# Kernel optimization log

Hardware: AMD Instinct MI355X
Metric: run time of the kernel (lower is better)

Reference implementation:

```python
import jax, jax.numpy as jnp
import numpy as np

N_NODES = 40000
N_EDGES = 640000
IN_DIM = 256
HID = 128
EMB = 128


def _mean_agg(h, src, dst, n):
    # PyG SimpleConv(aggr='mean'): out[i] = mean_{(j->i) in E} h[j]; 0 if no in-edges
    s = jax.ops.segment_sum(h[src], dst, num_segments=n)              # [N, D]
    deg = jax.ops.segment_sum(jnp.ones((src.shape[0],), h.dtype), dst,
                              num_segments=n)                          # [N]
    return s / jnp.maximum(deg, 1.0)[:, None]


def setup_inputs() -> dict:
    key = jax.random.key(0)
    ks = jax.random.split(key, 10)
    scale_in = 1.0 / np.sqrt(IN_DIM)
    scale_mix = 1.0 / np.sqrt(2 * HID)
    scale_out = 1.0 / np.sqrt(HID)
    return {
        "x": jax.random.normal(ks[0], (N_NODES, IN_DIM), dtype=jnp.float32),
        "W_in": jax.random.uniform(ks[1], (IN_DIM, HID), jnp.float32, -scale_in, scale_in),
        "b_in": jnp.zeros((HID,), jnp.float32),
        "W_mix0": jax.random.uniform(ks[2], (2 * HID, HID), jnp.float32, -scale_mix, scale_mix),
        "b_mix0": jnp.zeros((HID,), jnp.float32),
        "W_mix1": jax.random.uniform(ks[3], (2 * HID, HID), jnp.float32, -scale_mix, scale_mix),
        "b_mix1": jnp.zeros((HID,), jnp.float32),
        "W_out": jax.random.uniform(ks[4], (HID, EMB), jnp.float32, -scale_out, scale_out),
        "b_out": jnp.zeros((EMB,), jnp.float32),
        "edge_index": jax.random.randint(ks[5], (2, N_EDGES), 0, N_NODES, dtype=jnp.int64 if jax.config.jax_enable_x64 else jnp.int32),
    }


def reference(x, W_in, b_in, W_mix0, b_mix0, W_mix1, b_mix1, W_out, b_out, edge_index):
    src, dst = edge_index[0], edge_index[1]
    n = x.shape[0]
    # eval mode: dropout is identity
    h = jax.nn.relu(x @ W_in + b_in)                                   # [N, HID]
    for i, (W_mix, b_mix) in enumerate([(W_mix0, b_mix0), (W_mix1, b_mix1)]):
        h1 = _mean_agg(h, src, dst, n)                                 # 1-hop mean
        h2 = _mean_agg(h1, src, dst, n)                                # 2-hop mean
        h = jnp.concatenate([h1, h2], axis=-1) @ W_mix + b_mix         # [N, HID]
        if i != 1:
            h = jax.nn.relu(h)
    return h @ W_out + b_out                                           # [N, EMB]
```

## Files before the change

### kernel.cpp

```cpp
#include <hip/hip_runtime.h>

#define N_NODES 40000
#define N_EDGES 640000
#define IN_DIM 256
#define HID 128
#define NBUCK 313

typedef short bf16x8 __attribute__((ext_vector_type(8)));
typedef float f32x4 __attribute__((ext_vector_type(4)));

__device__ __forceinline__ unsigned short f2bf(float f) {
    unsigned int u = __float_as_uint(f);
    unsigned int r = (u + 0x7FFFu + ((u >> 16) & 1u)) >> 16;
    return (unsigned short)r;
}
__device__ __forceinline__ float bf2f(unsigned short b) {
    return __uint_as_float(((unsigned int)b) << 16);
}


__global__ __launch_bounds__(256) void count_prep(
    const int* __restrict__ dst, int* __restrict__ gbcnt, int E,
    const float* __restrict__ W0, const float* __restrict__ W1,
    const float* __restrict__ W2, const float* __restrict__ W3,
    unsigned short* __restrict__ H0, unsigned short* __restrict__ L0,
    unsigned short* __restrict__ H1, unsigned short* __restrict__ L1,
    unsigned short* __restrict__ H2, unsigned short* __restrict__ L2,
    unsigned short* __restrict__ H3, unsigned short* __restrict__ L3) {
    int bid = blockIdx.x, tid = threadIdx.x;
    if (bid < 157) {
        __shared__ int cnt[NBUCK];
        for (int j = tid; j < NBUCK; j += 256) cnt[j] = 0;
        __syncthreads();
        int base = bid * 4096;
        int lim = min(base + 4096, E);
        for (int i = base + tid; i < lim; i += 256) atomicAdd(&cnt[dst[i] >> 7], 1);
        __syncthreads();
        for (int j = tid; j < NBUCK; j += 256)
            if (cnt[j]) atomicAdd(&gbcnt[j], cnt[j]);
        return;
    }
    int i = (bid - 157) * 256 + tid;
    const float* W;
    unsigned short *H, *L;
    int local;
    if (i < 32768)       { W = W0; H = H0; L = L0; local = i; }
    else if (i < 65536)  { W = W1; H = H1; L = L1; local = i - 32768; }
    else if (i < 98304)  { W = W2; H = H2; L = L2; local = i - 65536; }
    else if (i < 114688) { W = W3; H = H3; L = L3; local = i - 98304; }
    else return;
    int k = local >> 7, c = local & 127;
    float w = W[local];
    unsigned short h = f2bf(w);
    unsigned short l = f2bf(w - bf2f(h));
    int d = (k >> 5) * 4096 + c * 32 + (k & 31);
    H[d] = h;
    L[d] = l;
}


__global__ __launch_bounds__(512) void scan_buckets(const int* __restrict__ gbcnt,
                                                    int* __restrict__ bbase,
                                                    int* __restrict__ bcursor,
                                                    int* __restrict__ row_off) {
    __shared__ int sh[512];
    int tid = threadIdx.x;
    int v = (tid < NBUCK) ? gbcnt[tid] : 0;
    sh[tid] = v;
    __syncthreads();
#pragma unroll
    for (int off = 1; off < 512; off <<= 1) {
        int t = (tid >= off) ? sh[tid - off] : 0;
        __syncthreads();
        sh[tid] += t;
        __syncthreads();
    }
    int excl = sh[tid] - v;
    if (tid < NBUCK) {
        bbase[tid] = excl;
        bcursor[tid] = excl;
    }
    if (tid == NBUCK - 1) bbase[NBUCK] = excl + v;
    if (tid == 0) row_off[N_NODES] = N_EDGES;
}


__global__ __launch_bounds__(256) void scatter_gemm1(
    const int* __restrict__ src, const int* __restrict__ dst,
    int* __restrict__ bcursor, unsigned int* __restrict__ stage, int E,
    const float* __restrict__ x,
    const unsigned short* __restrict__ Bth, const unsigned short* __restrict__ Btl,
    const float* __restrict__ bias, unsigned short* __restrict__ Cbf) {
    int bid = blockIdx.x;
    int tid = threadIdx.x;
    if (bid >= 625) {
        __shared__ int cnt[NBUCK];
        int b2 = bid - 625;
        for (int j = tid; j < NBUCK; j += 256) cnt[j] = 0;
        __syncthreads();
        int base = b2 * 4096;
        int lim = min(base + 4096, E);
        for (int i = base + tid; i < lim; i += 256) atomicAdd(&cnt[dst[i] >> 7], 1);
        __syncthreads();
        for (int j = tid; j < NBUCK; j += 256) {
            int c = cnt[j];
            if (c) cnt[j] = atomicAdd(&bcursor[j], c);
        }
        __syncthreads();
        for (int i = base + tid; i < lim; i += 256) {
            unsigned int d = (unsigned int)dst[i];
            int p = atomicAdd(&cnt[d >> 7], 1);
            stage[p] = (d << 16) | (unsigned int)src[i];
        }
        return;
    }
    __shared__ unsigned short Ah[64 * 32], Al[64 * 32];
    __shared__ unsigned short Bh[128 * 32], Bl[128 * 32];
    int lane = tid & 63, wid = tid >> 6;
    int wr = wid >> 1, wc = wid & 1;
    int row0 = bid * 64;

    f32x4 acc[2][4];
#pragma unroll
    for (int rt = 0; rt < 2; ++rt)
#pragma unroll
        for (int ct = 0; ct < 4; ++ct) acc[rt][ct] = 0.f;

    for (int s = 0; s < 8; ++s) {
        int kbase = s * 32;
#pragma unroll
        for (int i = 0; i < 2; ++i) {
            int cch = tid + i * 256;
            int r = cch >> 3, q = cch & 7;
            float4 v = *(const float4*)&x[(size_t)(row0 + r) * IN_DIM + kbase + q * 4];
            ushort4 hh, ll;
            hh.x = f2bf(v.x); ll.x = f2bf(v.x - bf2f(hh.x));
            hh.y = f2bf(v.y); ll.y = f2bf(v.y - bf2f(hh.y));
            hh.z = f2bf(v.z); ll.z = f2bf(v.z - bf2f(hh.z));
            hh.w = f2bf(v.w); ll.w = f2bf(v.w - bf2f(hh.w));
            *(ushort4*)&Ah[r * 32 + q * 4] = hh;
            *(ushort4*)&Al[r * 32 + q * 4] = ll;
        }
        {
            const float4* sh4 = (const float4*)(Bth + s * 4096);
            const float4* sl4 = (const float4*)(Btl + s * 4096);
            float4* dh4 = (float4*)Bh;
            float4* dl4 = (float4*)Bl;
            dh4[tid] = sh4[tid];
            dh4[tid + 256] = sh4[tid + 256];
            dl4[tid] = sl4[tid];
            dl4[tid + 256] = sl4[tid + 256];
        }
        __syncthreads();

        bf16x8 afh[2], afl[2], bfh[4], bfl[4];
#pragma unroll
        for (int rt = 0; rt < 2; ++rt) {
            int off = (wr * 32 + rt * 16 + (lane & 15)) * 32 + (lane >> 4) * 8;
            afh[rt] = *(const bf16x8*)&Ah[off];
            afl[rt] = *(const bf16x8*)&Al[off];
        }
#pragma unroll
        for (int ct = 0; ct < 4; ++ct) {
            int off = (wc * 64 + ct * 16 + (lane & 15)) * 32 + (lane >> 4) * 8;
            bfh[ct] = *(const bf16x8*)&Bh[off];
            bfl[ct] = *(const bf16x8*)&Bl[off];
        }
#pragma unroll
        for (int rt = 0; rt < 2; ++rt)
#pragma unroll
            for (int ct = 0; ct < 4; ++ct) {
                acc[rt][ct] = __builtin_amdgcn_mfma_f32_16x16x32_bf16(afh[rt], bfh[ct], acc[rt][ct], 0, 0, 0);
                acc[rt][ct] = __builtin_amdgcn_mfma_f32_16x16x32_bf16(afh[rt], bfl[ct], acc[rt][ct], 0, 0, 0);
                acc[rt][ct] = __builtin_amdgcn_mfma_f32_16x16x32_bf16(afl[rt], bfh[ct], acc[rt][ct], 0, 0, 0);
            }
        __syncthreads();
    }

#pragma unroll
    for (int ct = 0; ct < 4; ++ct) {
        int col = wc * 64 + ct * 16 + (lane & 15);
        float bv = bias[col];
#pragma unroll
        for (int rt = 0; rt < 2; ++rt) {
#pragma unroll
            for (int r = 0; r < 4; ++r) {
                int row = row0 + wr * 32 + rt * 16 + (lane >> 4) * 4 + r;
                float v = fmaxf(acc[rt][ct][r] + bv, 0.f);
                Cbf[(size_t)row * 128 + col] = f2bf(v);
            }
        }
    }
}


__global__ __launch_bounds__(256) void finalize_csr(const unsigned int* __restrict__ stage,
                                                    const int* __restrict__ bbase,
                                                    int* __restrict__ row_off,
                                                    int* __restrict__ csr) {
    __shared__ int ncnt[128];
    __shared__ int s2[128];
    int b = blockIdx.x, tid = threadIdx.x;
    int nbase = b << 7;
    int ncount = min(128, N_NODES - nbase);
    int ebase = bbase[b], eend = bbase[b + 1];
    if (tid < 128) ncnt[tid] = 0;
    __syncthreads();
    for (int i = ebase + tid; i < eend; i += 256)
        atomicAdd(&ncnt[(stage[i] >> 16) & 127], 1);
    __syncthreads();
    if (tid < 128) s2[tid] = ncnt[tid];
    __syncthreads();
#pragma unroll
    for (int off = 1; off < 128; off <<= 1) {
        int t = (tid < 128 && tid >= off) ? s2[tid - off] : 0;
        __syncthreads();
        if (tid < 128) s2[tid] += t;
        __syncthreads();
    }
    if (tid < 128) {
        int excl = s2[tid] - ncnt[tid];
        if (tid < ncount) row_off[nbase + tid] = ebase + excl;
        ncnt[tid] = excl;
    }
    __syncthreads();
    for (int i = ebase + tid; i < eend; i += 256) {
        unsigned int ent = stage[i];
        int loc = (ent >> 16) & 127;
        int p = atomicAdd(&ncnt[loc], 1);
        csr[ebase + p] = (int)(ent & 0xFFFFu);
    }
}


__global__ __launch_bounds__(256) void agg_mean_bf(const unsigned short* __restrict__ hbf,
                                                   const int* __restrict__ row_off,
                                                   const int* __restrict__ csr,
                                                   unsigned short* __restrict__ out_bf,
                                                   int N) {
    int node = blockIdx.x * 4 + (threadIdx.x >> 6);
    if (node >= N) return;
    int lane = threadIdx.x & 63;
    int half = lane >> 5;
    int sub = lane & 31;
    int beg = row_off[node], end = row_off[node + 1];
    float4 a0 = make_float4(0.f, 0.f, 0.f, 0.f);
    float4 a1 = make_float4(0.f, 0.f, 0.f, 0.f);
    int e = beg;
    for (; e + 7 < end; e += 8) {
        int s0 = csr[e + half];
        int s1 = csr[e + 2 + half];
        int s2 = csr[e + 4 + half];
        int s3 = csr[e + 6 + half];
        ushort4 u0 = *(const ushort4*)&hbf[(size_t)s0 * HID + sub * 4];
        ushort4 u1 = *(const ushort4*)&hbf[(size_t)s1 * HID + sub * 4];
        ushort4 u2 = *(const ushort4*)&hbf[(size_t)s2 * HID + sub * 4];
        ushort4 u3 = *(const ushort4*)&hbf[(size_t)s3 * HID + sub * 4];
        a0.x += bf2f(u0.x) + bf2f(u2.x);
        a0.y += bf2f(u0.y) + bf2f(u2.y);
        a0.z += bf2f(u0.z) + bf2f(u2.z);
        a0.w += bf2f(u0.w) + bf2f(u2.w);
        a1.x += bf2f(u1.x) + bf2f(u3.x);
        a1.y += bf2f(u1.y) + bf2f(u3.y);
        a1.z += bf2f(u1.z) + bf2f(u3.z);
        a1.w += bf2f(u1.w) + bf2f(u3.w);
    }
    for (; e + half < end; e += 2) {
        int s = csr[e + half];
        ushort4 u = *(const ushort4*)&hbf[(size_t)s * HID + sub * 4];
        a0.x += bf2f(u.x);
        a0.y += bf2f(u.y);
        a0.z += bf2f(u.z);
        a0.w += bf2f(u.w);
    }
    float4 acc;
    acc.x = a0.x + a1.x;
    acc.y = a0.y + a1.y;
    acc.z = a0.z + a1.z;
    acc.w = a0.w + a1.w;
    acc.x += __shfl_xor(acc.x, 32);
    acc.y += __shfl_xor(acc.y, 32);
    acc.z += __shfl_xor(acc.z, 32);
    acc.w += __shfl_xor(acc.w, 32);
    if (half == 0) {
        float inv = 1.0f / fmaxf((float)(end - beg), 1.0f);
        ushort4 ub;
        ub.x = f2bf(acc.x * inv);
        ub.y = f2bf(acc.y * inv);
        ub.z = f2bf(acc.z * inv);
        ub.w = f2bf(acc.w * inv);
        *(ushort4*)&out_bf[(size_t)node * HID + sub * 4] = ub;
    }
}


template <bool RELU>
__global__ __launch_bounds__(256) void gemm_a16(
    const unsigned short* __restrict__ A0, const unsigned short* __restrict__ A1,
    const unsigned short* __restrict__ Bth, const unsigned short* __restrict__ Btl,
    const float* __restrict__ bias, unsigned short* __restrict__ Cbf) {
    __shared__ unsigned short Ab[64 * 32];
    __shared__ unsigned short Bh[128 * 32], Bl[128 * 32];
    int tid = threadIdx.x;
    int lane = tid & 63, wid = tid >> 6;
    int wr = wid >> 1, wc = wid & 1;
    int row0 = blockIdx.x * 64;

    f32x4 acc[2][4];
#pragma unroll
    for (int rt = 0; rt < 2; ++rt)
#pragma unroll
        for (int ct = 0; ct < 4; ++ct) acc[rt][ct] = 0.f;

    for (int s = 0; s < 8; ++s) {
        const unsigned short* Asrc = (s < 4) ? A0 : A1;
        int kbase = (s & 3) * 32;
        {
            int r = tid >> 2, q = (tid & 3) * 8;
            *(float4*)&Ab[r * 32 + q] =
                *(const float4*)&Asrc[(size_t)(row0 + r) * HID + kbase + q];
        }
        {
            const float4* sh4 = (const float4*)(Bth + s * 4096);
            const float4* sl4 = (const float4*)(Btl + s * 4096);
            float4* dh4 = (float4*)Bh;
            float4* dl4 = (float4*)Bl;
            dh4[tid] = sh4[tid];
            dh4[tid + 256] = sh4[tid + 256];
            dl4[tid] = sl4[tid];
            dl4[tid + 256] = sl4[tid + 256];
        }
        __syncthreads();

        bf16x8 af[2], bfh[4], bfl[4];
#pragma unroll
        for (int rt = 0; rt < 2; ++rt) {
            int off = (wr * 32 + rt * 16 + (lane & 15)) * 32 + (lane >> 4) * 8;
            af[rt] = *(const bf16x8*)&Ab[off];
        }
#pragma unroll
        for (int ct = 0; ct < 4; ++ct) {
            int off = (wc * 64 + ct * 16 + (lane & 15)) * 32 + (lane >> 4) * 8;
            bfh[ct] = *(const bf16x8*)&Bh[off];
            bfl[ct] = *(const bf16x8*)&Bl[off];
        }
#pragma unroll
        for (int rt = 0; rt < 2; ++rt)
#pragma unroll
            for (int ct = 0; ct < 4; ++ct) {
                acc[rt][ct] = __builtin_amdgcn_mfma_f32_16x16x32_bf16(af[rt], bfh[ct], acc[rt][ct], 0, 0, 0);
                acc[rt][ct] = __builtin_amdgcn_mfma_f32_16x16x32_bf16(af[rt], bfl[ct], acc[rt][ct], 0, 0, 0);
            }
        __syncthreads();
    }

#pragma unroll
    for (int ct = 0; ct < 4; ++ct) {
        int col = wc * 64 + ct * 16 + (lane & 15);
        float bv = bias[col];
#pragma unroll
        for (int rt = 0; rt < 2; ++rt) {
#pragma unroll
            for (int r = 0; r < 4; ++r) {
                int row = row0 + wr * 32 + rt * 16 + (lane >> 4) * 4 + r;
                float v = acc[rt][ct][r] + bv;
                if (RELU) v = fmaxf(v, 0.f);
                Cbf[(size_t)row * 128 + col] = f2bf(v);
            }
        }
    }
}


__global__ __launch_bounds__(256) void gemm_mix_out(
    const unsigned short* __restrict__ A0, const unsigned short* __restrict__ A1,
    const unsigned short* __restrict__ BmH, const unsigned short* __restrict__ BmL,
    const float* __restrict__ bias_m,
    const unsigned short* __restrict__ BoH, const unsigned short* __restrict__ BoL,
    const float* __restrict__ bias_o, float* __restrict__ out) {
    __shared__ unsigned short Ab[64 * 32];
    __shared__ unsigned short Bh[128 * 32], Bl[128 * 32];
    __shared__ unsigned short AoH[4][64 * 32], AoL[4][64 * 32];
    int tid = threadIdx.x;
    int lane = tid & 63, wid = tid >> 6;
    int wr = wid >> 1, wc = wid & 1;
    int row0 = blockIdx.x * 64;

    f32x4 acc[2][4];
#pragma unroll
    for (int rt = 0; rt < 2; ++rt)
#pragma unroll
        for (int ct = 0; ct < 4; ++ct) acc[rt][ct] = 0.f;

    for (int s = 0; s < 8; ++s) {
        const unsigned short* Asrc = (s < 4) ? A0 : A1;
        int kbase = (s & 3) * 32;
        {
            int r = tid >> 2, q = (tid & 3) * 8;
            *(float4*)&Ab[r * 32 + q] =
                *(const float4*)&Asrc[(size_t)(row0 + r) * HID + kbase + q];
        }
        {
            const float4* sh4 = (const float4*)(BmH + s * 4096);
            const float4* sl4 = (const float4*)(BmL + s * 4096);
            float4* dh4 = (float4*)Bh;
            float4* dl4 = (float4*)Bl;
            dh4[tid] = sh4[tid];
            dh4[tid + 256] = sh4[tid + 256];
            dl4[tid] = sl4[tid];
            dl4[tid + 256] = sl4[tid + 256];
        }
        __syncthreads();

        bf16x8 af[2], bfh[4], bfl[4];
#pragma unroll
        for (int rt = 0; rt < 2; ++rt) {
            int off = (wr * 32 + rt * 16 + (lane & 15)) * 32 + (lane >> 4) * 8;
            af[rt] = *(const bf16x8*)&Ab[off];
        }
#pragma unroll
        for (int ct = 0; ct < 4; ++ct) {
            int off = (wc * 64 + ct * 16 + (lane & 15)) * 32 + (lane >> 4) * 8;
            bfh[ct] = *(const bf16x8*)&Bh[off];
            bfl[ct] = *(const bf16x8*)&Bl[off];
        }
#pragma unroll
        for (int rt = 0; rt < 2; ++rt)
#pragma unroll
            for (int ct = 0; ct < 4; ++ct) {
                acc[rt][ct] = __builtin_amdgcn_mfma_f32_16x16x32_bf16(af[rt], bfh[ct], acc[rt][ct], 0, 0, 0);
                acc[rt][ct] = __builtin_amdgcn_mfma_f32_16x16x32_bf16(af[rt], bfl[ct], acc[rt][ct], 0, 0, 0);
            }
        __syncthreads();
    }

#pragma unroll
    for (int ct = 0; ct < 4; ++ct) {
        int c = wc * 64 + ct * 16 + (lane & 15);
        int sp = c >> 5, cc = c & 31;
        float bv = bias_m[c];
#pragma unroll
        for (int rt = 0; rt < 2; ++rt) {
#pragma unroll
            for (int r = 0; r < 4; ++r) {
                int rl = wr * 32 + rt * 16 + (lane >> 4) * 4 + r;
                float v = acc[rt][ct][r] + bv;
                unsigned short h = f2bf(v);
                unsigned short l = f2bf(v - bf2f(h));
                AoH[sp][rl * 32 + cc] = h;
                AoL[sp][rl * 32 + cc] = l;
            }
        }
    }

#pragma unroll
    for (int rt = 0; rt < 2; ++rt)
#pragma unroll
        for (int ct = 0; ct < 4; ++ct) acc[rt][ct] = 0.f;

    for (int s = 0; s < 4; ++s) {
        {
            const float4* sh4 = (const float4*)(BoH + s * 4096);
            const float4* sl4 = (const float4*)(BoL + s * 4096);
            float4* dh4 = (float4*)Bh;
            float4* dl4 = (float4*)Bl;
            dh4[tid] = sh4[tid];
            dh4[tid + 256] = sh4[tid + 256];
            dl4[tid] = sl4[tid];
            dl4[tid + 256] = sl4[tid + 256];
        }
        __syncthreads();

        bf16x8 afh[2], afl[2], bfh[4], bfl[4];
#pragma unroll
        for (int rt = 0; rt < 2; ++rt) {
            int off = (wr * 32 + rt * 16 + (lane & 15)) * 32 + (lane >> 4) * 8;
            afh[rt] = *(const bf16x8*)&AoH[s][off];
            afl[rt] = *(const bf16x8*)&AoL[s][off];
        }
#pragma unroll
        for (int ct = 0; ct < 4; ++ct) {
            int off = (wc * 64 + ct * 16 + (lane & 15)) * 32 + (lane >> 4) * 8;
            bfh[ct] = *(const bf16x8*)&Bh[off];
            bfl[ct] = *(const bf16x8*)&Bl[off];
        }
#pragma unroll
        for (int rt = 0; rt < 2; ++rt)
#pragma unroll
            for (int ct = 0; ct < 4; ++ct) {
                acc[rt][ct] = __builtin_amdgcn_mfma_f32_16x16x32_bf16(afh[rt], bfh[ct], acc[rt][ct], 0, 0, 0);
                acc[rt][ct] = __builtin_amdgcn_mfma_f32_16x16x32_bf16(afh[rt], bfl[ct], acc[rt][ct], 0, 0, 0);
                acc[rt][ct] = __builtin_amdgcn_mfma_f32_16x16x32_bf16(afl[rt], bfh[ct], acc[rt][ct], 0, 0, 0);
            }
        __syncthreads();
    }

#pragma unroll
    for (int ct = 0; ct < 4; ++ct) {
        int col = wc * 64 + ct * 16 + (lane & 15);
        float bv = bias_o[col];
#pragma unroll
        for (int rt = 0; rt < 2; ++rt) {
#pragma unroll
            for (int r = 0; r < 4; ++r) {
                int row = row0 + wr * 32 + rt * 16 + (lane >> 4) * 4 + r;
                out[(size_t)row * 128 + col] = acc[rt][ct][r] + bv;
            }
        }
    }
}


extern "C" void kernel_launch(void* const* d_in, const int* in_sizes, int n_in,
                              void* d_out, int out_size, void* d_ws, size_t ws_size,
                              hipStream_t stream) {
    const float* x     = (const float*)d_in[0];
    const float* W_in  = (const float*)d_in[1];
    const float* b_in  = (const float*)d_in[2];
    const float* W_m0  = (const float*)d_in[3];
    const float* b_m0  = (const float*)d_in[4];
    const float* W_m1  = (const float*)d_in[5];
    const float* b_m1  = (const float*)d_in[6];
    const float* W_o   = (const float*)d_in[7];
    const float* b_o   = (const float*)d_in[8];
    const int*   eidx  = (const int*)d_in[9];
    const int* src = eidx;
    const int* dst = eidx + N_EDGES;

    char* ws = (char*)d_ws;
    size_t off = 0;
    auto alloc = [&](size_t bytes) -> char* {
        char* p = ws + off;
        off += (bytes + 255) & ~(size_t)255;
        return p;
    };
    int* gbcnt   = (int*)alloc((size_t)NBUCK * 4);
    int* bbase   = (int*)alloc((size_t)(NBUCK + 1) * 4);
    int* bcursor = (int*)alloc((size_t)NBUCK * 4);
    int* row_off = (int*)alloc((size_t)(N_NODES + 1) * 4);
    int* csr     = (int*)alloc((size_t)N_EDGES * 4);
    unsigned int* stage = (unsigned int*)alloc((size_t)N_EDGES * 4);
    unsigned short* hbf1 = (unsigned short*)alloc((size_t)N_NODES * HID * 2);
    unsigned short* hbf2 = (unsigned short*)alloc((size_t)N_NODES * HID * 2);
    unsigned short* hbf3 = (unsigned short*)alloc((size_t)N_NODES * HID * 2);
    unsigned short* WinH = (unsigned short*)alloc(32768 * 2);
    unsigned short* WinL = (unsigned short*)alloc(32768 * 2);
    unsigned short* Wm0H = (unsigned short*)alloc(32768 * 2);
    unsigned short* Wm0L = (unsigned short*)alloc(32768 * 2);
    unsigned short* Wm1H = (unsigned short*)alloc(32768 * 2);
    unsigned short* Wm1L = (unsigned short*)alloc(32768 * 2);
    unsigned short* WoH  = (unsigned short*)alloc(16384 * 2);
    unsigned short* WoL  = (unsigned short*)alloc(16384 * 2);
    (void)ws_size;

    hipMemsetAsync(gbcnt, 0, (size_t)NBUCK * 4, stream);
    count_prep<<<157 + 448, 256, 0, stream>>>(dst, gbcnt, N_EDGES,
                                              W_in, W_m0, W_m1, W_o,
                                              WinH, WinL, Wm0H, Wm0L,
                                              Wm1H, Wm1L, WoH, WoL);
    scan_buckets<<<1, 512, 0, stream>>>(gbcnt, bbase, bcursor, row_off);
    scatter_gemm1<<<625 + 157, 256, 0, stream>>>(src, dst, bcursor, stage, N_EDGES,
                                                 x, WinH, WinL, b_in, hbf1);
    finalize_csr<<<NBUCK, 256, 0, stream>>>(stage, bbase, row_off, csr);

    agg_mean_bf<<<10000, 256, 0, stream>>>(hbf1, row_off, csr, hbf2, N_NODES);
    agg_mean_bf<<<10000, 256, 0, stream>>>(hbf2, row_off, csr, hbf3, N_NODES);
    gemm_a16<true><<<625, 256, 0, stream>>>(hbf2, hbf3, Wm0H, Wm0L, b_m0, hbf1);

    agg_mean_bf<<<10000, 256, 0, stream>>>(hbf1, row_off, csr, hbf2, N_NODES);
    agg_mean_bf<<<10000, 256, 0, stream>>>(hbf2, row_off, csr, hbf3, N_NODES);

    gemm_mix_out<<<625, 256, 0, stream>>>(hbf2, hbf3, Wm1H, Wm1L, b_m1,
                                          WoH, WoL, b_o, (float*)d_out);
}
```

Measured before the change: 187.9 us.

## Replace global bucket atomics and scan kernel with per-block count table

Count blocks now write their per-bucket histograms to a per-block table instead of atomically accumulating global counts. Each scatter block recomputes bucket totals and its own prefix offsets from that table, which removes the memset, the single-block scan kernel and the global cursor atomics. This cuts two launches and makes the scatter order deterministic. In exchange, every scatter block reads the whole 157x313 table and runs a serial 313-step scan on one thread.

Measured after the change: 184.3 us. Within noise of the previous version (-1.9%).

```diff
diff --git a/kernel.cpp b/kernel.cpp
--- a/kernel.cpp
+++ b/kernel.cpp
@@ -5,6 +5,8 @@
 #define IN_DIM 256
 #define HID 128
 #define NBUCK 313
+#define NCB 157
+#define PBS 320
 
 typedef short bf16x8 __attribute__((ext_vector_type(8)));
 typedef float f32x4 __attribute__((ext_vector_type(4)));
@@ -20,7 +22,7 @@
 
 
 __global__ __launch_bounds__(256) void count_prep(
-    const int* __restrict__ dst, int* __restrict__ gbcnt, int E,
+    const int* __restrict__ dst, int* __restrict__ pbcnt, int E,
     const float* __restrict__ W0, const float* __restrict__ W1,
     const float* __restrict__ W2, const float* __restrict__ W3,
     unsigned short* __restrict__ H0, unsigned short* __restrict__ L0,
@@ -28,7 +30,7 @@
     unsigned short* __restrict__ H2, unsigned short* __restrict__ L2,
     unsigned short* __restrict__ H3, unsigned short* __restrict__ L3) {
     int bid = blockIdx.x, tid = threadIdx.x;
-    if (bid < 157) {
+    if (bid < NCB) {
         __shared__ int cnt[NBUCK];
         for (int j = tid; j < NBUCK; j += 256) cnt[j] = 0;
         __syncthreads();
@@ -36,11 +38,10 @@
         int lim = min(base + 4096, E);
         for (int i = base + tid; i < lim; i += 256) atomicAdd(&cnt[dst[i] >> 7], 1);
         __syncthreads();
-        for (int j = tid; j < NBUCK; j += 256)
-            if (cnt[j]) atomicAdd(&gbcnt[j], cnt[j]);
+        for (int j = tid; j < NBUCK; j += 256) pbcnt[bid * PBS + j] = cnt[j];
         return;
     }
-    int i = (bid - 157) * 256 + tid;
+    int i = (bid - NCB) * 256 + tid;
     const float* W;
     unsigned short *H, *L;
     int local;
@@ -59,54 +60,48 @@
 }
 
 
-__global__ __launch_bounds__(512) void scan_buckets(const int* __restrict__ gbcnt,
-                                                    int* __restrict__ bbase,
-                                                    int* __restrict__ bcursor,
-                                                    int* __restrict__ row_off) {
-    __shared__ int sh[512];
-    int tid = threadIdx.x;
-    int v = (tid < NBUCK) ? gbcnt[tid] : 0;
-    sh[tid] = v;
-    __syncthreads();
-#pragma unroll
-    for (int off = 1; off < 512; off <<= 1) {
-        int t = (tid >= off) ? sh[tid - off] : 0;
-        __syncthreads();
-        sh[tid] += t;
-        __syncthreads();
-    }
-    int excl = sh[tid] - v;
-    if (tid < NBUCK) {
-        bbase[tid] = excl;
-        bcursor[tid] = excl;
-    }
-    if (tid == NBUCK - 1) bbase[NBUCK] = excl + v;
-    if (tid == 0) row_off[N_NODES] = N_EDGES;
-}
-
-
 __global__ __launch_bounds__(256) void scatter_gemm1(
     const int* __restrict__ src, const int* __restrict__ dst,
-    int* __restrict__ bcursor, unsigned int* __restrict__ stage, int E,
+    const int* __restrict__ pbcnt, int* __restrict__ bbase, int* __restrict__ row_off,
+    unsigned int* __restrict__ stage, int E,
     const float* __restrict__ x,
     const unsigned short* __restrict__ Bth, const unsigned short* __restrict__ Btl,
     const float* __restrict__ bias, unsigned short* __restrict__ Cbf) {
     int bid = blockIdx.x;
     int tid = threadIdx.x;
     if (bid >= 625) {
-        __shared__ int cnt[NBUCK];
+        __shared__ int tot[NBUCK], par[NBUCK], bb[NBUCK], cnt[NBUCK];
         int b2 = bid - 625;
-        for (int j = tid; j < NBUCK; j += 256) cnt[j] = 0;
+        for (int j = tid; j < NBUCK; j += 256) {
+            int t = 0, p = 0;
+            for (int blk = 0; blk < NCB; ++blk) {
+                int c = pbcnt[blk * PBS + j];
+                t += c;
+                if (blk < b2) p += c;
+            }
+            tot[j] = t;
+            par[j] = p;
+        }
+        __syncthreads();
+        if (tid == 0) {
+            int running = 0;
+            for (int j = 0; j < NBUCK; ++j) {
+                bb[j] = running;
+                running += tot[j];
+            }
+        }
+        __syncthreads();
+        for (int j = tid; j < NBUCK; j += 256) {
+            cnt[j] = bb[j] + par[j];
+            if (b2 == 0) bbase[j] = bb[j];
+        }
+        if (b2 == 0 && tid == 0) {
+            bbase[NBUCK] = N_EDGES;
+            row_off[N_NODES] = N_EDGES;
+        }
         __syncthreads();
         int base = b2 * 4096;
         int lim = min(base + 4096, E);
-        for (int i = base + tid; i < lim; i += 256) atomicAdd(&cnt[dst[i] >> 7], 1);
-        __syncthreads();
-        for (int j = tid; j < NBUCK; j += 256) {
-            int c = cnt[j];
-            if (c) cnt[j] = atomicAdd(&bcursor[j], c);
-        }
-        __syncthreads();
         for (int i = base + tid; i < lim; i += 256) {
             unsigned int d = (unsigned int)dst[i];
             int p = atomicAdd(&cnt[d >> 7], 1);
@@ -534,9 +529,8 @@
         off += (bytes + 255) & ~(size_t)255;
         return p;
     };
-    int* gbcnt   = (int*)alloc((size_t)NBUCK * 4);
+    int* pbcnt   = (int*)alloc((size_t)NCB * PBS * 4);
     int* bbase   = (int*)alloc((size_t)(NBUCK + 1) * 4);
-    int* bcursor = (int*)alloc((size_t)NBUCK * 4);
     int* row_off = (int*)alloc((size_t)(N_NODES + 1) * 4);
     int* csr     = (int*)alloc((size_t)N_EDGES * 4);
     unsigned int* stage = (unsigned int*)alloc((size_t)N_EDGES * 4);
@@ -553,13 +547,12 @@
     unsigned short* WoL  = (unsigned short*)alloc(16384 * 2);
     (void)ws_size;
 
-    hipMemsetAsync(gbcnt, 0, (size_t)NBUCK * 4, stream);
-    count_prep<<<157 + 448, 256, 0, stream>>>(dst, gbcnt, N_EDGES,
+    count_prep<<<NCB + 448, 256, 0, stream>>>(dst, pbcnt, N_EDGES,
                                               W_in, W_m0, W_m1, W_o,
                                               WinH, WinL, Wm0H, Wm0L,
                                               Wm1H, Wm1L, WoH, WoL);
-    scan_buckets<<<1, 512, 0, stream>>>(gbcnt, bbase, bcursor, row_off);
-    scatter_gemm1<<<625 + 157, 256, 0, stream>>>(src, dst, bcursor, stage, N_EDGES,
+    scatter_gemm1<<<625 + NCB, 256, 0, stream>>>(src, dst, pbcnt, bbase, row_off,
+                                                 stage, N_EDGES,
                                                  x, WinH, WinL, b_in, hbf1);
     finalize_csr<<<NBUCK, 256, 0, stream>>>(stage, bbase, row_off, csr);
 
```
